# Kernel tuning notes

Measured on AMD Instinct MI355X. Metric: run time of the kernel, lower is better.

The kernel has to match this reference:

```python
import jax, jax.numpy as jnp
import numpy as np

N_NODES = 100000
N_EDGES = 1250000
IN_DIM = 12
HID = 64
N_LAYERS = 3
LN_EPS = 1e-5
LEAKY_SLOPE = 0.01


def _layer_norm(x, g, b):
    mu = jnp.mean(x, axis=-1, keepdims=True)
    var = jnp.var(x, axis=-1, keepdims=True)
    return (x - mu) * jax.lax.rsqrt(var + LN_EPS) * g + b


def setup_inputs() -> dict:
    key = jax.random.key(0)
    ks = jax.random.split(key, 16)
    s = 0.1  # param init scale
    return {
        "x": jax.random.normal(ks[0], (N_NODES, IN_DIM), jnp.float32),
        "edge_index": jax.random.randint(ks[1], (2, N_EDGES), 0, N_NODES, jnp.int64),
        "edge_weight": jax.random.uniform(ks[2], (N_EDGES,), jnp.float32),
        "in_W": s * jax.random.normal(ks[3], (IN_DIM, HID), jnp.float32),
        "in_b": jnp.zeros((HID,), jnp.float32),
        "lin_W": s * jax.random.normal(ks[4], (N_LAYERS, HID, HID), jnp.float32),
        "lin_b": jnp.zeros((N_LAYERS, HID), jnp.float32),
        "att_W": s * jax.random.normal(ks[5], (N_LAYERS, 2 * HID, 1), jnp.float32),
        "att_b": jnp.zeros((N_LAYERS, 1), jnp.float32),
        "ln_g": jnp.ones((N_LAYERS, HID), jnp.float32),
        "ln_b": jnp.zeros((N_LAYERS, HID), jnp.float32),
        "out1_W": s * jax.random.normal(ks[6], (HID, HID // 2), jnp.float32),
        "out1_b": jnp.zeros((HID // 2,), jnp.float32),
        "out2_W": s * jax.random.normal(ks[7], (HID // 2, 1), jnp.float32),
        "out2_b": jnp.zeros((1,), jnp.float32),
    }


def reference(x, edge_index, edge_weight, in_W, in_b, lin_W, lin_b,
              att_W, att_b, ln_g, ln_b, out1_W, out1_b, out2_W, out2_b):
    row, col = edge_index[0], edge_index[1]
    h = x @ in_W + in_b  # [N, HID]
    for i in range(N_LAYERS):
        hl = h @ lin_W[i] + lin_b[i]  # [N, HID]
        h_i = hl[row]  # [E, HID]
        h_j = hl[col]  # [E, HID]
        att_in = jnp.concatenate([h_i, h_j], axis=-1)  # [E, 2*HID]
        scores = jax.nn.leaky_relu(att_in @ att_W[i] + att_b[i], LEAKY_SLOPE)  # [E, 1]
        scores = jax.nn.softmax(scores, axis=0)  # global softmax over edges (as in source)
        scores = scores * edge_weight[:, None]
        messages = scores * h_j  # [E, HID]
        agg = jax.ops.segment_sum(messages, row, num_segments=N_NODES)
        h_new = jax.nn.relu(hl + agg)
        h_new = _layer_norm(h_new, ln_g[i], ln_b[i])
        # dropout is identity in eval mode
        h = h + h_new
    z = jax.nn.relu(h @ out1_W + out1_b)
    return jax.nn.sigmoid(z @ out2_W + out2_b)  # [N, 1]
```

## Files before the change

kernel.cpp:

```cpp
#include <hip/hip_runtime.h>
#include <hip/hip_fp8.h>
#include <math.h>

#define N_NODES 100000
#define N_EDGES 1250000
#define IN_DIM 12
#define HID 64
#define N_LAYERS 3
#define LN_EPS 1e-5f
#define SLOPE 0.01f

#define NODE_BLOCKS ((N_NODES + 3) / 4)
#define EDGE_TBLOCKS ((N_EDGES + 255) / 256)
#define SCAN_BLOCKS ((N_NODES + 1023) / 1024)
#define MFMA_BLOCKS2 ((N_NODES + 127) / 128)
#define OUT_BLOCKS ((N_NODES + 63) / 64)
#define NEDGE_BLOCKS ((N_NODES + 255) / 256)

#define BUCKETS 256
#define BUCKET_NODES 391
#define P1_EDGES 4096
#define P1_BLOCKS ((N_EDGES + P1_EDGES - 1) / P1_EDGES)

#define LEW_SCALE 2048.0f
#define LEW_INV (1.0f / 2048.0f)

typedef short bf16x8 __attribute__((ext_vector_type(8)));
typedef float f32x4 __attribute__((ext_vector_type(4)));
typedef float f32x2 __attribute__((ext_vector_type(2)));

#if defined(__has_builtin)
#if __has_builtin(__builtin_amdgcn_cvt_pk_f32_fp8)
#define HAVE_PK_FP8 1
#endif
#endif

static __device__ __forceinline__ unsigned short f2bf(float f) {
  union { float f; unsigned int u; } v; v.f = f;
  unsigned int r = v.u + 0x7FFFu + ((v.u >> 16) & 1u);
  return (unsigned short)(r >> 16);
}
static __device__ __forceinline__ unsigned char f2e4(float f) {
  return __hip_fp8_e4m3(f).__x;
}
static __device__ __forceinline__ float e42f(unsigned char b) {
  __hip_fp8_e4m3 d; d.__x = b;
  return (float)d;
}

__global__ void k_in_proj(const float* __restrict__ x,
                          const float* __restrict__ W,
                          const float* __restrict__ b,
                          float* __restrict__ h) {
  __shared__ float sW[IN_DIM * HID];
  for (int i = threadIdx.x; i < IN_DIM * HID; i += blockDim.x) sW[i] = W[i];
  __syncthreads();
  int wave = threadIdx.x >> 6, lane = threadIdx.x & 63;
  int n = blockIdx.x * 4 + wave;
  if (n >= N_NODES) return;
  float acc = b[lane];
#pragma unroll
  for (int k = 0; k < IN_DIM; ++k)
    acc += x[n * IN_DIM + k] * sW[k * HID + lane];
  h[n * HID + lane] = acc;
}

__global__ void k_hist(const int* __restrict__ ei, int* __restrict__ deg) {
  int e = blockIdx.x * 256 + threadIdx.x;
  if (e >= N_EDGES) return;
  atomicAdd(&deg[ei[e]], 1);
}

__global__ void k_blocksums(const int* __restrict__ deg, int* __restrict__ bsum) {
  __shared__ int sm[1024];
  int i = blockIdx.x * 1024 + threadIdx.x;
  sm[threadIdx.x] = (i < N_NODES) ? deg[i] : 0;
  __syncthreads();
  for (int st = 512; st > 0; st >>= 1) {
    if (threadIdx.x < st) sm[threadIdx.x] += sm[threadIdx.x + st];
    __syncthreads();
  }
  if (threadIdx.x == 0) bsum[blockIdx.x] = sm[0];
}

__global__ void k_scan_bsums(int* __restrict__ bsum, int nb) {
  __shared__ int sm[128];
  int v = (threadIdx.x < nb) ? bsum[threadIdx.x] : 0;
  sm[threadIdx.x] = v;
  __syncthreads();
  for (int st = 1; st < 128; st <<= 1) {
    int t = (threadIdx.x >= st) ? sm[threadIdx.x - st] : 0;
    __syncthreads();
    sm[threadIdx.x] += t;
    __syncthreads();
  }
  if (threadIdx.x < nb) bsum[threadIdx.x] = sm[threadIdx.x] - v;
}

__global__ void k_scan_final(const int* __restrict__ deg, const int* __restrict__ bsum,
                             int* __restrict__ rowptr, unsigned* __restrict__ gbcur) {
  __shared__ int sm[1024];
  int i = blockIdx.x * 1024 + threadIdx.x;
  int v = (i < N_NODES) ? deg[i] : 0;
  sm[threadIdx.x] = v;
  __syncthreads();
  for (int st = 1; st < 1024; st <<= 1) {
    int t = (threadIdx.x >= st) ? sm[threadIdx.x - st] : 0;
    __syncthreads();
    sm[threadIdx.x] += t;
    __syncthreads();
  }
  int excl = sm[threadIdx.x] - v + bsum[blockIdx.x];
  if (i < N_NODES) {
    rowptr[i] = excl;
    int bb = i / BUCKET_NODES;
    if (i - bb * BUCKET_NODES == 0) gbcur[bb] = (unsigned)excl;
  }
}

__global__ void k_fill_p1(const int* __restrict__ ei, const float* __restrict__ ew,
                          unsigned* __restrict__ gbcur,
                          unsigned long long* __restrict__ tmp) {
  __shared__ unsigned cnt[BUCKETS], gbase[BUCKETS], lofs[BUCKETS];
  int t = threadIdx.x;
  cnt[t] = 0;
  __syncthreads();
  int base = blockIdx.x * P1_EDGES;
#pragma unroll
  for (int i = 0; i < 16; ++i) {
    int e = base + i * 256 + t;
    if (e < N_EDGES) atomicAdd(&cnt[(unsigned)ei[e] / BUCKET_NODES], 1u);
  }
  __syncthreads();
  {
    unsigned c = cnt[t];
    gbase[t] = c ? atomicAdd(&gbcur[t], c) : 0u;
    lofs[t] = 0;
  }
  __syncthreads();
#pragma unroll
  for (int i = 0; i < 16; ++i) {
    int e = base + i * 256 + t;
    if (e < N_EDGES) {
      unsigned r = (unsigned)ei[e], c = (unsigned)ei[N_EDGES + e];
      float lew = __logf(ew[e]);
      lew = fmaxf(lew, -15.9995f);
      unsigned q = (unsigned)(-lew * LEW_SCALE + 0.5f);
      if (q > 32767u) q = 32767u;
      unsigned b = r / BUCKET_NODES;
      unsigned idx = atomicAdd(&lofs[b], 1u);
      tmp[gbase[b] + idx] = ((unsigned long long)r << 32)
                          | ((unsigned long long)c << 15) | q;
    }
  }
}

__global__ void k_fill_p2(const int* __restrict__ rowptr,
                          const unsigned long long* __restrict__ tmp,
                          unsigned* __restrict__ packed) {
  __shared__ int lcur[BUCKET_NODES];
  int b = blockIdx.x, t = threadIdx.x;
  int nb0 = b * BUCKET_NODES;
  int nb1 = min(nb0 + BUCKET_NODES, N_NODES);
  int nn = nb1 - nb0;
  for (int j = t; j < nn; j += 256) lcur[j] = rowptr[nb0 + j];
  __syncthreads();
  int beg = rowptr[nb0];
  int end = (nb1 < N_NODES) ? rowptr[nb1] : N_EDGES;
  for (int i = beg + t; i < end; i += 256) {
    unsigned long long rec = tmp[i];
    int r = (int)(rec >> 32);
    int pos = atomicAdd(&lcur[r - nb0], 1);
    packed[pos] = (unsigned)(rec & 0xFFFFFFFFu);
  }
}

__global__ void k_prep(const float* __restrict__ lin_W,
                       const float* __restrict__ lin_b,
                       const float* __restrict__ att_W,
                       float* __restrict__ uvec,
                       float* __restrict__ ucst) {
  int l = blockIdx.x, j = threadIdx.x;
  const float* Wl = lin_W + l * HID * HID;
  const float* a1 = att_W + l * 2 * HID;
  const float* a2 = a1 + HID;
  float s1 = 0.f, s2 = 0.f;
  for (int c = 0; c < HID; ++c) {
    float w = Wl[j * HID + c];
    s1 += w * a1[c];
    s2 += w * a2[c];
  }
  uvec[l * 128 + j] = s1;
  uvec[l * 128 + 64 + j] = s2;
  float t1 = lin_b[l * HID + j] * a1[j];
  float t2 = lin_b[l * HID + j] * a2[j];
#pragma unroll
  for (int off = 32; off > 0; off >>= 1) {
    t1 += __shfl_xor(t1, off, 64);
    t2 += __shfl_xor(t2, off, 64);
  }
  if (j == 0) { ucst[l * 2] = t1; ucst[l * 2 + 1] = t2; }
}

__global__ void k_lin_mfma(const float* __restrict__ h,
                           const float* __restrict__ W,
                           const float* __restrict__ bias,
                           const float* __restrict__ uvec,
                           const float* __restrict__ ucst,
                           float* __restrict__ hl,
                           unsigned char* __restrict__ hl8,
                           float* __restrict__ alpha1,
                           float* __restrict__ alpha2) {
  __shared__ unsigned short Wt[HID * 72];
  for (int idx = threadIdx.x; idx < HID * HID; idx += 256) {
    int k = idx >> 6, n = idx & 63;
    Wt[n * 72 + k] = f2bf(W[idx]);
  }
  __syncthreads();

  int wave = threadIdx.x >> 6, lane = threadIdx.x & 63;
  int g = lane >> 4, r = lane & 15;

#pragma unroll
  for (int tile = 0; tile < 2; ++tile) {
    int nb = blockIdx.x * 128 + tile * 64 + wave * 16;
    int row = nb + r;
    bool rowok = row < N_NODES;
    if (nb >= N_NODES) break;

    f32x4 f0 = {0,0,0,0}, f1 = {0,0,0,0}, f2v = {0,0,0,0}, f3 = {0,0,0,0};
    if (rowok) {
      const float* hrow = h + (size_t)row * HID;
      f0  = *(const f32x4*)(hrow + g * 8);
      f1  = *(const f32x4*)(hrow + g * 8 + 4);
      f2v = *(const f32x4*)(hrow + 32 + g * 8);
      f3  = *(const f32x4*)(hrow + 32 + g * 8 + 4);
    }
    bf16x8 a0, a1f;
#pragma unroll
    for (int i = 0; i < 4; ++i) {
      a0[i]      = (short)f2bf(f0[i]);
      a0[i + 4]  = (short)f2bf(f1[i]);
      a1f[i]     = (short)f2bf(f2v[i]);
      a1f[i + 4] = (short)f2bf(f3[i]);
    }

    f32x4 acc[4] = {{0,0,0,0},{0,0,0,0},{0,0,0,0},{0,0,0,0}};
#pragma unroll
    for (int nt = 0; nt < 4; ++nt) {
      bf16x8 b0 = *(const bf16x8*)&Wt[(nt * 16 + r) * 72 + g * 8];
      bf16x8 b1 = *(const bf16x8*)&Wt[(nt * 16 + r) * 72 + 32 + g * 8];
      acc[nt] = __builtin_amdgcn_mfma_f32_16x16x32_bf16(a0, b0, acc[nt], 0, 0, 0);
      acc[nt] = __builtin_amdgcn_mfma_f32_16x16x32_bf16(a1f, b1, acc[nt], 0, 0, 0);
    }

    {
      const float* u1 = uvec;
      const float* u2 = uvec + HID;
      f32x4 ua = *(const f32x4*)(u1 + g * 8),      ub = *(const f32x4*)(u1 + g * 8 + 4);
      f32x4 uc = *(const f32x4*)(u1 + 32 + g * 8), ud = *(const f32x4*)(u1 + 32 + g * 8 + 4);
      float p1 = f0[0]*ua[0]+f0[1]*ua[1]+f0[2]*ua[2]+f0[3]*ua[3]
               + f1[0]*ub[0]+f1[1]*ub[1]+f1[2]*ub[2]+f1[3]*ub[3]
               + f2v[0]*uc[0]+f2v[1]*uc[1]+f2v[2]*uc[2]+f2v[3]*uc[3]
               + f3[0]*ud[0]+f3[1]*ud[1]+f3[2]*ud[2]+f3[3]*ud[3];
      ua = *(const f32x4*)(u2 + g * 8);      ub = *(const f32x4*)(u2 + g * 8 + 4);
      uc = *(const f32x4*)(u2 + 32 + g * 8); ud = *(const f32x4*)(u2 + 32 + g * 8 + 4);
      float p2 = f0[0]*ua[0]+f0[1]*ua[1]+f0[2]*ua[2]+f0[3]*ua[3]
               + f1[0]*ub[0]+f1[1]*ub[1]+f1[2]*ub[2]+f1[3]*ub[3]
               + f2v[0]*uc[0]+f2v[1]*uc[1]+f2v[2]*uc[2]+f2v[3]*uc[3]
               + f3[0]*ud[0]+f3[1]*ud[1]+f3[2]*ud[2]+f3[3]*ud[3];
      p1 += __shfl_xor(p1, 16, 64); p1 += __shfl_xor(p1, 32, 64);
      p2 += __shfl_xor(p2, 16, 64); p2 += __shfl_xor(p2, 32, 64);
      if (g == 0 && rowok) {
        alpha1[row] = p1 + ucst[0];
        alpha2[row] = p2 + ucst[1];
      }
    }

#pragma unroll
    for (int nt = 0; nt < 4; ++nt) {
      float bv = bias[nt * 16 + r];
#pragma unroll
      for (int reg = 0; reg < 4; ++reg) {
        int n2 = nb + g * 4 + reg;
        if (n2 < N_NODES) {
          float v = acc[nt][reg] + bv;
          hl[(size_t)n2 * HID + nt * 16 + r] = v;
          hl8[(size_t)n2 * HID + nt * 16 + r] = f2e4(v);
        }
      }
    }
  }
}

__global__ void k_edge(const int* __restrict__ rowptr,
                       const int* __restrict__ deg,
                       const unsigned* __restrict__ packed,
                       const float* __restrict__ alpha1,
                       const float* __restrict__ alpha2,
                       const float* __restrict__ attB,
                       float* __restrict__ slw,
                       float* __restrict__ pmax,
                       float* __restrict__ psum,
                       int* __restrict__ counter,
                       float* __restrict__ red) {
  int t = threadIdx.x;
  int n = blockIdx.x * 256 + t;
  float m = -INFINITY, sum = 0.f;
  if (n < N_NODES) {
    float a1 = alpha1[n] + attB[0];
    int beg = rowptr[n];
    int end = beg + deg[n];
    for (int p = beg; p < end; ++p) {
      unsigned u = packed[p];
      float sc = a1 + alpha2[u >> 15];
      sc = sc > 0.f ? sc : SLOPE * sc;
      slw[p] = sc - (float)(u & 0x7FFFu) * LEW_INV;
      if (sc > m) { sum *= __expf(m - sc); m = sc; }
      sum += __expf(sc - m);
    }
  }
  __shared__ float smax[256], ssum[256];
  __shared__ bool last;
  smax[t] = m; ssum[t] = sum;
  __syncthreads();
  for (int st = 128; st > 0; st >>= 1) {
    if (t < st) {
      float ma = smax[t], mb = smax[t + st];
      float sa = ssum[t], sb = ssum[t + st];
      float mm = fmaxf(ma, mb);
      float ss = 0.f;
      if (mm != -INFINITY)
        ss = (ma == -INFINITY ? 0.f : sa * __expf(ma - mm))
           + (mb == -INFINITY ? 0.f : sb * __expf(mb - mm));
      smax[t] = mm; ssum[t] = ss;
    }
    __syncthreads();
  }
  if (t == 0) {
    pmax[blockIdx.x] = smax[0];
    psum[blockIdx.x] = ssum[0];
    __threadfence();
    int old = atomicAdd(counter, 1);
    last = (old == (int)gridDim.x - 1);
  }
  __syncthreads();
  if (!last) return;
  __threadfence();
  volatile const float* vpm = pmax;
  volatile const float* vps = psum;
  float m2 = -INFINITY, s2 = 0.f;
  for (int i = t; i < (int)gridDim.x; i += 256) {
    float mb = vpm[i], sb = vps[i];
    if (mb != -INFINITY) {
      if (mb > m2) { s2 *= __expf(m2 - mb); m2 = mb; }
      s2 += sb * __expf(mb - m2);
    }
  }
  __syncthreads();
  smax[t] = m2; ssum[t] = s2;
  __syncthreads();
  for (int st = 128; st > 0; st >>= 1) {
    if (t < st) {
      float ma = smax[t], mb = smax[t + st];
      float sa = ssum[t], sb = ssum[t + st];
      float mm = fmaxf(ma, mb);
      float ss = 0.f;
      if (mm != -INFINITY)
        ss = (ma == -INFINITY ? 0.f : sa * __expf(ma - mm))
           + (mb == -INFINITY ? 0.f : sb * __expf(mb - mm));
      smax[t] = mm; ssum[t] = ss;
    }
    __syncthreads();
  }
  if (t == 0) {
    red[0] = smax[0];
    red[1] = ssum[0];
    *counter = 0;
  }
}

__global__ void k_exp2(f32x4* __restrict__ slw, const float* __restrict__ red) {
  int i = blockIdx.x * 256 + threadIdx.x;
  int nvec = (N_EDGES + 3) / 4;
  if (i >= nvec) return;
  float M = red[0];
  f32x4 v = slw[i];
  v[0] = __expf(v[0] - M);
  v[1] = __expf(v[1] - M);
  v[2] = __expf(v[2] - M);
  v[3] = __expf(v[3] - M);
  slw[i] = v;
}

__global__ void k_agg_update(const int* __restrict__ rowptr,
                             const int* __restrict__ deg,
                             const unsigned* __restrict__ packed,
                             const float* __restrict__ w,
                             const float* __restrict__ red,
                             const float* __restrict__ hl,
                             const unsigned char* __restrict__ hl8,
                             const float* __restrict__ gam,
                             const float* __restrict__ bet,
                             float* __restrict__ h) {
  int wave = threadIdx.x >> 6, lane = threadIdx.x & 63;
  int n = blockIdx.x * 4 + wave;
  if (n >= N_NODES) return;
  int g = lane >> 4, q = lane & 15;
  int beg = rowptr[n];
  int end = beg + deg[n];

  float a0 = 0.f, a1 = 0.f, a2 = 0.f, a3 = 0.f;
  for (int k = beg; k < end; k += 16) {
    int ke0 = k + g, ke1 = k + 4 + g, ke2 = k + 8 + g, ke3 = k + 12 + g;
    bool v0 = ke0 < end, v1 = ke1 < end, v2 = ke2 < end, v3 = ke3 < end;
    unsigned u0 = packed[v0 ? ke0 : beg];
    unsigned u1 = packed[v1 ? ke1 : beg];
    unsigned u2 = packed[v2 ? ke2 : beg];
    unsigned u3 = packed[v3 ? ke3 : beg];
    float w0 = v0 ? w[ke0] : 0.f;
    float w1 = v1 ? w[ke1] : 0.f;
    float w2 = v2 ? w[ke2] : 0.f;
    float w3 = v3 ? w[ke3] : 0.f;
    unsigned d0 = *(const unsigned*)(hl8 + (size_t)(u0 >> 15) * HID + q * 4);
    unsigned d1 = *(const unsigned*)(hl8 + (size_t)(u1 >> 15) * HID + q * 4);
    unsigned d2 = *(const unsigned*)(hl8 + (size_t)(u2 >> 15) * HID + q * 4);
    unsigned d3 = *(const unsigned*)(hl8 + (size_t)(u3 >> 15) * HID + q * 4);
#ifdef HAVE_PK_FP8
    f32x2 l0 = __builtin_amdgcn_cvt_pk_f32_fp8((int)d0, 0);
    f32x2 h0 = __builtin_amdgcn_cvt_pk_f32_fp8((int)d0, 1);
    f32x2 l1 = __builtin_amdgcn_cvt_pk_f32_fp8((int)d1, 0);
    f32x2 h1 = __builtin_amdgcn_cvt_pk_f32_fp8((int)d1, 1);
    f32x2 l2 = __builtin_amdgcn_cvt_pk_f32_fp8((int)d2, 0);
    f32x2 h2 = __builtin_amdgcn_cvt_pk_f32_fp8((int)d2, 1);
    f32x2 l3 = __builtin_amdgcn_cvt_pk_f32_fp8((int)d3, 0);
    f32x2 h3 = __builtin_amdgcn_cvt_pk_f32_fp8((int)d3, 1);
    a0 += w0 * l0[0] + w1 * l1[0] + w2 * l2[0] + w3 * l3[0];
    a1 += w0 * l0[1] + w1 * l1[1] + w2 * l2[1] + w3 * l3[1];
    a2 += w0 * h0[0] + w1 * h1[0] + w2 * h2[0] + w3 * h3[0];
    a3 += w0 * h0[1] + w1 * h1[1] + w2 * h2[1] + w3 * h3[1];
#else
    a0 += w0 * e42f(d0 & 0xffu) + w1 * e42f(d1 & 0xffu)
        + w2 * e42f(d2 & 0xffu) + w3 * e42f(d3 & 0xffu);
    a1 += w0 * e42f((d0 >> 8) & 0xffu) + w1 * e42f((d1 >> 8) & 0xffu)
        + w2 * e42f((d2 >> 8) & 0xffu) + w3 * e42f((d3 >> 8) & 0xffu);
    a2 += w0 * e42f((d0 >> 16) & 0xffu) + w1 * e42f((d1 >> 16) & 0xffu)
        + w2 * e42f((d2 >> 16) & 0xffu) + w3 * e42f((d3 >> 16) & 0xffu);
    a3 += w0 * e42f(d0 >> 24) + w1 * e42f(d1 >> 24)
        + w2 * e42f(d2 >> 24) + w3 * e42f(d3 >> 24);
#endif
  }
  a0 += __shfl_xor(a0, 16, 64); a0 += __shfl_xor(a0, 32, 64);
  a1 += __shfl_xor(a1, 16, 64); a1 += __shfl_xor(a1, 32, 64);
  a2 += __shfl_xor(a2, 16, 64); a2 += __shfl_xor(a2, 32, 64);
  a3 += __shfl_xor(a3, 16, 64); a3 += __shfl_xor(a3, 32, 64);

  float inv = 1.0f / red[1];
  const float* hlrow = hl + (size_t)n * HID + q * 4;
  float v0 = fmaxf(hlrow[0] + a0 * inv, 0.f);
  float v1 = fmaxf(hlrow[1] + a1 * inv, 0.f);
  float v2 = fmaxf(hlrow[2] + a2 * inv, 0.f);
  float v3 = fmaxf(hlrow[3] + a3 * inv, 0.f);

  float ms = v0 + v1 + v2 + v3;
  ms += __shfl_xor(ms, 1, 64); ms += __shfl_xor(ms, 2, 64);
  ms += __shfl_xor(ms, 4, 64); ms += __shfl_xor(ms, 8, 64);
  float m = ms * (1.0f / HID);
  float d0 = v0 - m, d1 = v1 - m, d2 = v2 - m, d3 = v3 - m;
  float vs = d0 * d0 + d1 * d1 + d2 * d2 + d3 * d3;
  vs += __shfl_xor(vs, 1, 64); vs += __shfl_xor(vs, 2, 64);
  vs += __shfl_xor(vs, 4, 64); vs += __shfl_xor(vs, 8, 64);
  float rs = rsqrtf(vs * (1.0f / HID) + LN_EPS);

  if (g == 0) {
    float* hrow = h + (size_t)n * HID + q * 4;
    f32x4 hv = *(const f32x4*)hrow;
    f32x4 gv = *(const f32x4*)(gam + q * 4);
    f32x4 bv = *(const f32x4*)(bet + q * 4);
    f32x4 o;
    o[0] = hv[0] + d0 * rs * gv[0] + bv[0];
    o[1] = hv[1] + d1 * rs * gv[1] + bv[1];
    o[2] = hv[2] + d2 * rs * gv[2] + bv[2];
    o[3] = hv[3] + d3 * rs * gv[3] + bv[3];
    *(f32x4*)hrow = o;
  }
}

__global__ void k_out_mfma(const float* __restrict__ h,
                           const float* __restrict__ W1,
                           const float* __restrict__ b1,
                           const float* __restrict__ W2,
                           const float* __restrict__ b2,
                           float* __restrict__ out) {
  __shared__ unsigned short W1t[32 * 72];
  __shared__ float sW2[32];
  for (int idx = threadIdx.x; idx < HID * 32; idx += 256) {
    int k = idx >> 5, m = idx & 31;
    W1t[m * 72 + k] = f2bf(W1[idx]);
  }
  if (threadIdx.x < 32) sW2[threadIdx.x] = W2[threadIdx.x];
  __syncthreads();

  int wave = threadIdx.x >> 6, lane = threadIdx.x & 63;
  int g = lane >> 4, r = lane & 15;
  int nb = blockIdx.x * 64 + wave * 16;
  int row = nb + r;
  bool rowok = row < N_NODES;

  f32x4 f0 = {0,0,0,0}, f1 = {0,0,0,0}, f2v = {0,0,0,0}, f3 = {0,0,0,0};
  if (rowok) {
    const float* hrow = h + (size_t)row * HID;
    f0  = *(const f32x4*)(hrow + g * 8);
    f1  = *(const f32x4*)(hrow + g * 8 + 4);
    f2v = *(const f32x4*)(hrow + 32 + g * 8);
    f3  = *(const f32x4*)(hrow + 32 + g * 8 + 4);
  }
  bf16x8 a0, a1f;
#pragma unroll
  for (int i = 0; i < 4; ++i) {
    a0[i]      = (short)f2bf(f0[i]);
    a0[i + 4]  = (short)f2bf(f1[i]);
    a1f[i]     = (short)f2bf(f2v[i]);
    a1f[i + 4] = (short)f2bf(f3[i]);
  }

  f32x4 acc[2] = {{0,0,0,0},{0,0,0,0}};
#pragma unroll
  for (int mt = 0; mt < 2; ++mt) {
    bf16x8 b0 = *(const bf16x8*)&W1t[(mt * 16 + r) * 72 + g * 8];
    bf16x8 b1v = *(const bf16x8*)&W1t[(mt * 16 + r) * 72 + 32 + g * 8];
    acc[mt] = __builtin_amdgcn_mfma_f32_16x16x32_bf16(a0, b0, acc[mt], 0, 0, 0);
    acc[mt] = __builtin_amdgcn_mfma_f32_16x16x32_bf16(a1f, b1v, acc[mt], 0, 0, 0);
  }

  float part[4];
#pragma unroll
  for (int reg = 0; reg < 4; ++reg) {
    float p = 0.f;
#pragma unroll
    for (int mt = 0; mt < 2; ++mt) {
      float z = acc[mt][reg] + b1[mt * 16 + r];
      p += fmaxf(z, 0.f) * sW2[mt * 16 + r];
    }
    p += __shfl_xor(p, 1, 64);
    p += __shfl_xor(p, 2, 64);
    p += __shfl_xor(p, 4, 64);
    p += __shfl_xor(p, 8, 64);
    part[reg] = p;
  }
  if (r == 0) {
    float bb = b2[0];
#pragma unroll
    for (int reg = 0; reg < 4; ++reg) {
      int n2 = nb + g * 4 + reg;
      if (n2 < N_NODES)
        out[n2] = 1.0f / (1.0f + expf(-(part[reg] + bb)));
    }
  }
}

extern "C" void kernel_launch(void* const* d_in, const int* in_sizes, int n_in,
                              void* d_out, int out_size, void* d_ws, size_t ws_size,
                              hipStream_t stream) {
  const float* x      = (const float*)d_in[0];
  const int*   ei     = (const int*)d_in[1];
  const float* ew     = (const float*)d_in[2];
  const float* in_W   = (const float*)d_in[3];
  const float* in_b   = (const float*)d_in[4];
  const float* lin_W  = (const float*)d_in[5];
  const float* lin_b  = (const float*)d_in[6];
  const float* att_W  = (const float*)d_in[7];
  const float* att_b  = (const float*)d_in[8];
  const float* ln_g   = (const float*)d_in[9];
  const float* ln_b   = (const float*)d_in[10];
  const float* out1_W = (const float*)d_in[11];
  const float* out1_b = (const float*)d_in[12];
  const float* out2_W = (const float*)d_in[13];
  const float* out2_b = (const float*)d_in[14];
  float* out = (float*)d_out;

  float* ws = (float*)d_ws;
  float* h            = ws;
  float* hl           = ws + 6400000;
  unsigned char* hl8  = (unsigned char*)(ws + 12800000);
  unsigned long long* tmp = (unsigned long long*)(ws + 14500000);
  unsigned* packed    = (unsigned*)(ws + 17000000);
  float* slw          = ws + 18250000;
  int* deg            = (int*)(ws + 19500000);
  int* counter        = deg + N_NODES;
  int* rowptr         = (int*)(ws + 19601000);
  float* alpha1       = ws + 19702000;
  float* alpha2       = ws + 19803000;
  float* pmax         = ws + 19904000;
  float* psum         = ws + 19906000;
  float* red          = ws + 19908000;
  float* uvec         = ws + 19909000;
  float* ucst         = ws + 19910000;
  int* bsum           = (int*)(ws + 19911000);
  unsigned* gbcur     = (unsigned*)(ws + 19912000);

  hipMemsetAsync(deg, 0, (N_NODES + 1) * sizeof(int), stream);
  k_hist<<<EDGE_TBLOCKS, 256, 0, stream>>>(ei, deg);
  k_blocksums<<<SCAN_BLOCKS, 1024, 0, stream>>>(deg, bsum);
  k_scan_bsums<<<1, 128, 0, stream>>>(bsum, SCAN_BLOCKS);
  k_scan_final<<<SCAN_BLOCKS, 1024, 0, stream>>>(deg, bsum, rowptr, gbcur);
  k_fill_p1<<<P1_BLOCKS, 256, 0, stream>>>(ei, ew, gbcur, tmp);
  k_fill_p2<<<BUCKETS, 256, 0, stream>>>(rowptr, tmp, packed);

  k_prep<<<N_LAYERS, 64, 0, stream>>>(lin_W, lin_b, att_W, uvec, ucst);
  k_in_proj<<<NODE_BLOCKS, 256, 0, stream>>>(x, in_W, in_b, h);

  for (int i = 0; i < N_LAYERS; ++i) {
    k_lin_mfma<<<MFMA_BLOCKS2, 256, 0, stream>>>(h, lin_W + i * HID * HID, lin_b + i * HID,
                                                 uvec + i * 128, ucst + i * 2,
                                                 hl, hl8, alpha1, alpha2);
    k_edge<<<NEDGE_BLOCKS, 256, 0, stream>>>(rowptr, deg, packed, alpha1, alpha2,
                                             att_b + i, slw, pmax, psum, counter, red);
    k_exp2<<<(((N_EDGES + 3) / 4) + 255) / 256, 256, 0, stream>>>((f32x4*)slw, red);
    k_agg_update<<<NODE_BLOCKS, 256, 0, stream>>>(rowptr, deg, packed, slw, red,
                                                  hl, hl8, ln_g + i * HID, ln_b + i * HID, h);
  }

  k_out_mfma<<<OUT_BLOCKS, 256, 0, stream>>>(h, out1_W, out1_b, out2_W, out2_b, out);
}
```

Before: 430.9 us.

## Build CSR via bucket histogram and per-bucket local scan instead of global degree scan

Replaces the per-node global atomic degree histogram and three-kernel scan with a per-block bucket histogram, a single 256-entry bucket scan, and per-bucket local node histograms and scans inside the second fill pass, which now also writes rowptr. The deg array is dropped and consumers use rowptr[n+1]. This removes 1.25M global atomics and two launches from CSR construction. In exchange, fill_p2 reads tmp twice and uses 512-thread blocks, and correctness relies on BUCKET_NODES being at most 512.

Result: faster. 375.2 us (-12.9%).

```diff
diff --git a/kernel.cpp b/kernel.cpp
--- a/kernel.cpp
+++ b/kernel.cpp
@@ -12,7 +12,6 @@
 
 #define NODE_BLOCKS ((N_NODES + 3) / 4)
 #define EDGE_TBLOCKS ((N_EDGES + 255) / 256)
-#define SCAN_BLOCKS ((N_NODES + 1023) / 1024)
 #define MFMA_BLOCKS2 ((N_NODES + 127) / 128)
 #define OUT_BLOCKS ((N_NODES + 63) / 64)
 #define NEDGE_BLOCKS ((N_NODES + 255) / 256)
@@ -65,56 +64,42 @@
   h[n * HID + lane] = acc;
 }
 
-__global__ void k_hist(const int* __restrict__ ei, int* __restrict__ deg) {
-  int e = blockIdx.x * 256 + threadIdx.x;
-  if (e >= N_EDGES) return;
-  atomicAdd(&deg[ei[e]], 1);
-}
-
-__global__ void k_blocksums(const int* __restrict__ deg, int* __restrict__ bsum) {
-  __shared__ int sm[1024];
-  int i = blockIdx.x * 1024 + threadIdx.x;
-  sm[threadIdx.x] = (i < N_NODES) ? deg[i] : 0;
-  __syncthreads();
-  for (int st = 512; st > 0; st >>= 1) {
-    if (threadIdx.x < st) sm[threadIdx.x] += sm[threadIdx.x + st];
+__global__ void k_bhist(const int* __restrict__ ei, unsigned* __restrict__ bcnt) {
+  __shared__ unsigned cnt[BUCKETS];
+  int t = threadIdx.x;
+  cnt[t] = 0;
+  __syncthreads();
+  int base = blockIdx.x * P1_EDGES;
+#pragma unroll
+  for (int i = 0; i < 16; ++i) {
+    int e = base + i * 256 + t;
+    if (e < N_EDGES) atomicAdd(&cnt[(unsigned)ei[e] / BUCKET_NODES], 1u);
+  }
+  __syncthreads();
+  if (cnt[t]) atomicAdd(&bcnt[t], cnt[t]);
+}
+
+__global__ void k_bscan(const unsigned* __restrict__ bcnt,
+                        unsigned* __restrict__ boffs,
+                        unsigned* __restrict__ gbcur,
+                        int* __restrict__ rowptr) {
+  __shared__ unsigned sm[BUCKETS];
+  int t = threadIdx.x;
+  unsigned v = bcnt[t];
+  sm[t] = v;
+  __syncthreads();
+  for (int st = 1; st < BUCKETS; st <<= 1) {
+    unsigned tv = (t >= st) ? sm[t - st] : 0u;
     __syncthreads();
-  }
-  if (threadIdx.x == 0) bsum[blockIdx.x] = sm[0];
-}
-
-__global__ void k_scan_bsums(int* __restrict__ bsum, int nb) {
-  __shared__ int sm[128];
-  int v = (threadIdx.x < nb) ? bsum[threadIdx.x] : 0;
-  sm[threadIdx.x] = v;
-  __syncthreads();
-  for (int st = 1; st < 128; st <<= 1) {
-    int t = (threadIdx.x >= st) ? sm[threadIdx.x - st] : 0;
+    sm[t] += tv;
     __syncthreads();
-    sm[threadIdx.x] += t;
-    __syncthreads();
-  }
-  if (threadIdx.x < nb) bsum[threadIdx.x] = sm[threadIdx.x] - v;
-}
-
-__global__ void k_scan_final(const int* __restrict__ deg, const int* __restrict__ bsum,
-                             int* __restrict__ rowptr, unsigned* __restrict__ gbcur) {
-  __shared__ int sm[1024];
-  int i = blockIdx.x * 1024 + threadIdx.x;
-  int v = (i < N_NODES) ? deg[i] : 0;
-  sm[threadIdx.x] = v;
-  __syncthreads();
-  for (int st = 1; st < 1024; st <<= 1) {
-    int t = (threadIdx.x >= st) ? sm[threadIdx.x - st] : 0;
-    __syncthreads();
-    sm[threadIdx.x] += t;
-    __syncthreads();
-  }
-  int excl = sm[threadIdx.x] - v + bsum[blockIdx.x];
-  if (i < N_NODES) {
-    rowptr[i] = excl;
-    int bb = i / BUCKET_NODES;
-    if (i - bb * BUCKET_NODES == 0) gbcur[bb] = (unsigned)excl;
+  }
+  unsigned excl = sm[t] - v;
+  boffs[t] = excl;
+  gbcur[t] = excl;
+  if (t == 0) {
+    boffs[BUCKETS] = N_EDGES;
+    rowptr[N_NODES] = N_EDGES;
   }
 }
 
@@ -155,22 +140,41 @@
   }
 }
 
-__global__ void k_fill_p2(const int* __restrict__ rowptr,
+__global__ void k_fill_p2(const unsigned* __restrict__ boffs,
                           const unsigned long long* __restrict__ tmp,
+                          int* __restrict__ rowptr,
                           unsigned* __restrict__ packed) {
-  __shared__ int lcur[BUCKET_NODES];
+  __shared__ unsigned lhist[512];
+  __shared__ unsigned lcur[512];
   int b = blockIdx.x, t = threadIdx.x;
   int nb0 = b * BUCKET_NODES;
   int nb1 = min(nb0 + BUCKET_NODES, N_NODES);
   int nn = nb1 - nb0;
-  for (int j = t; j < nn; j += 256) lcur[j] = rowptr[nb0 + j];
-  __syncthreads();
-  int beg = rowptr[nb0];
-  int end = (nb1 < N_NODES) ? rowptr[nb1] : N_EDGES;
-  for (int i = beg + t; i < end; i += 256) {
+  int beg = (int)boffs[b];
+  int end = (int)boffs[b + 1];
+
+  lhist[t] = 0;
+  __syncthreads();
+  for (int i = beg + t; i < end; i += 512) {
+    int r = (int)(tmp[i] >> 32);
+    atomicAdd(&lhist[r - nb0], 1u);
+  }
+  __syncthreads();
+  unsigned degv = lhist[t];
+  for (int st = 1; st < 512; st <<= 1) {
+    unsigned tv = (t >= st) ? lhist[t - st] : 0u;
+    __syncthreads();
+    lhist[t] += tv;
+    __syncthreads();
+  }
+  unsigned excl = lhist[t] - degv;
+  if (t < nn) rowptr[nb0 + t] = beg + (int)excl;
+  lcur[t] = (unsigned)beg + excl;
+  __syncthreads();
+  for (int i = beg + t; i < end; i += 512) {
     unsigned long long rec = tmp[i];
     int r = (int)(rec >> 32);
-    int pos = atomicAdd(&lcur[r - nb0], 1);
+    unsigned pos = atomicAdd(&lcur[r - nb0], 1u);
     packed[pos] = (unsigned)(rec & 0xFFFFFFFFu);
   }
 }
@@ -294,7 +298,6 @@
 }
 
 __global__ void k_edge(const int* __restrict__ rowptr,
-                       const int* __restrict__ deg,
                        const unsigned* __restrict__ packed,
                        const float* __restrict__ alpha1,
                        const float* __restrict__ alpha2,
@@ -310,7 +313,7 @@
   if (n < N_NODES) {
     float a1 = alpha1[n] + attB[0];
     int beg = rowptr[n];
-    int end = beg + deg[n];
+    int end = rowptr[n + 1];
     for (int p = beg; p < end; ++p) {
       unsigned u = packed[p];
       float sc = a1 + alpha2[u >> 15];
@@ -394,7 +397,6 @@
 }
 
 __global__ void k_agg_update(const int* __restrict__ rowptr,
-                             const int* __restrict__ deg,
                              const unsigned* __restrict__ packed,
                              const float* __restrict__ w,
                              const float* __restrict__ red,
@@ -408,7 +410,7 @@
   if (n >= N_NODES) return;
   int g = lane >> 4, q = lane & 15;
   int beg = rowptr[n];
-  int end = beg + deg[n];
+  int end = rowptr[n + 1];
 
   float a0 = 0.f, a1 = 0.f, a2 = 0.f, a3 = 0.f;
   for (int k = beg; k < end; k += 16) {
@@ -586,9 +588,10 @@
   unsigned long long* tmp = (unsigned long long*)(ws + 14500000);
   unsigned* packed    = (unsigned*)(ws + 17000000);
   float* slw          = ws + 18250000;
-  int* deg            = (int*)(ws + 19500000);
-  int* counter        = deg + N_NODES;
-  int* rowptr         = (int*)(ws + 19601000);
+  int* rowptr         = (int*)(ws + 19500000);
+  int* counter        = (int*)(ws + 19601000);
+  unsigned* bcnt      = (unsigned*)(counter + 1);
+  unsigned* boffs     = bcnt + 256;
   float* alpha1       = ws + 19702000;
   float* alpha2       = ws + 19803000;
   float* pmax         = ws + 19904000;
@@ -596,16 +599,13 @@
   float* red          = ws + 19908000;
   float* uvec         = ws + 19909000;
   float* ucst         = ws + 19910000;
-  int* bsum           = (int*)(ws + 19911000);
   unsigned* gbcur     = (unsigned*)(ws + 19912000);
 
-  hipMemsetAsync(deg, 0, (N_NODES + 1) * sizeof(int), stream);
-  k_hist<<<EDGE_TBLOCKS, 256, 0, stream>>>(ei, deg);
-  k_blocksums<<<SCAN_BLOCKS, 1024, 0, stream>>>(deg, bsum);
-  k_scan_bsums<<<1, 128, 0, stream>>>(bsum, SCAN_BLOCKS);
-  k_scan_final<<<SCAN_BLOCKS, 1024, 0, stream>>>(deg, bsum, rowptr, gbcur);
+  hipMemsetAsync(counter, 0, (1 + 256) * sizeof(int), stream);
+  k_bhist<<<P1_BLOCKS, 256, 0, stream>>>(ei, bcnt);
+  k_bscan<<<1, 256, 0, stream>>>(bcnt, boffs, gbcur, rowptr);
   k_fill_p1<<<P1_BLOCKS, 256, 0, stream>>>(ei, ew, gbcur, tmp);
-  k_fill_p2<<<BUCKETS, 256, 0, stream>>>(rowptr, tmp, packed);
+  k_fill_p2<<<BUCKETS, 512, 0, stream>>>(boffs, tmp, rowptr, packed);
 
   k_prep<<<N_LAYERS, 64, 0, stream>>>(lin_W, lin_b, att_W, uvec, ucst);
   k_in_proj<<<NODE_BLOCKS, 256, 0, stream>>>(x, in_W, in_b, h);
@@ -614,10 +614,10 @@
     k_lin_mfma<<<MFMA_BLOCKS2, 256, 0, stream>>>(h, lin_W + i * HID * HID, lin_b + i * HID,
                                                  uvec + i * 128, ucst + i * 2,
                                                  hl, hl8, alpha1, alpha2);
-    k_edge<<<NEDGE_BLOCKS, 256, 0, stream>>>(rowptr, deg, packed, alpha1, alpha2,
+    k_edge<<<NEDGE_BLOCKS, 256, 0, stream>>>(rowptr, packed, alpha1, alpha2,
                                              att_b + i, slw, pmax, psum, counter, red);
     k_exp2<<<(((N_EDGES + 3) / 4) + 255) / 256, 256, 0, stream>>>((f32x4*)slw, red);
-    k_agg_update<<<NODE_BLOCKS, 256, 0, stream>>>(rowptr, deg, packed, slw, red,
+    k_agg_update<<<NODE_BLOCKS, 256, 0, stream>>>(rowptr, packed, slw, red,
                                                   hl, hl8, ln_g + i * HID, ln_b + i * HID, h);
   }
 
```
